# Optimization experiments

Measured on AMD Instinct MI355X. Metric: run time of the kernel, lower is better.

Reference implementation:

```python
import jax, jax.numpy as jnp
import numpy as np
from jax import lax

EPS = 1e-06


def _ema_scan(x, s):
    # x: [B, C, T]; s: [C] smoothing coeff in [0, 1]
    # Recurrence: y_0 = x_0; y_t = s * x_t + (1 - s) * y_{t-1}
    # Expressed as affine pairs (A_t, b_t) with y_t = A_t * y_{t-1} + b_t
    s_b = s[None, :, None]  # [1, C, 1]
    A0 = jnp.zeros_like(x[:, :, :1])
    A_rest = jnp.broadcast_to(1.0 - s_b, x[:, :, 1:].shape)
    A = jnp.concatenate([A0, A_rest], axis=2)
    b = jnp.concatenate([x[:, :, :1], s_b * x[:, :, 1:]], axis=2)

    def combine(c1, c2):
        a1, b1 = c1
        a2, b2 = c2
        return (a1 * a2, a2 * b1 + b2)

    _, ema = lax.associative_scan(combine, (A, b), axis=2)
    return ema


def setup_inputs() -> dict:
    key = jax.random.key(0)
    B, C, T = 32, 128, 16000
    kx, = jax.random.split(key, 1)
    x = jax.random.uniform(kx, (B, C, T), dtype=jnp.float32)
    alpha = jnp.ones((C,), dtype=jnp.float32) * 0.96
    delta = jnp.ones((C,), dtype=jnp.float32) * 2.0
    root = jnp.ones((C,), dtype=jnp.float32) * 2.0
    ema_weights = jnp.ones((C,), dtype=jnp.float32) * 0.04
    return {"x": x, "alpha": alpha, "delta": delta, "root": root, "ema_weights": ema_weights}


def reference(x, alpha, delta, root, ema_weights):
    # sPCEN: per-channel EMA smoother + power-law compression
    s = jnp.clip(ema_weights, 0.0, 1.0)
    ema = _ema_scan(x, s)  # [B, C, T]

    alpha_c = jnp.minimum(alpha, 1.0)[None, :, None]
    root_c = jnp.maximum(root, 1.0)[None, :, None]
    r = 1.0 / root_c
    d = delta[None, :, None]

    out = (x / (EPS + ema) ** alpha_c + d) ** r - d ** r
    return out
```

## Files before the change

kernel.cpp:

```cpp
#include <hip/hip_runtime.h>
#include <math.h>

#define T_LEN    16000
#define T_LEN4   4000
#define THREADS  256
#define CHUNK    16
#define TILE4    (THREADS * 4)
#define NT       4
#define EPS_F    1e-6f

__launch_bounds__(THREADS, 5)
__global__ void pcen_kernel(const float* __restrict__ x,
                            const float* __restrict__ alpha,
                            const float* __restrict__ delta,
                            const float* __restrict__ root,
                            const float* __restrict__ ema_w,
                            float* __restrict__ out, int C) {
    __shared__ float swA[2][4], swB[2][4];

    const int row  = blockIdx.x;
    const int c    = row % C;
    const int tid  = threadIdx.x;
    const int lane = tid & 63;
    const int wave = tid >> 6;

    const float s   = fminf(fmaxf(ema_w[c], 0.0f), 1.0f);
    const float q   = 1.0f - s;
    const float a_c = fminf(alpha[c], 1.0f);
    const float r   = 1.0f / fmaxf(root[c], 1.0f);
    const float d   = delta[c];
    const float dr  = powf(d, r);
    const float q16 = powf(q, (float)CHUNK);
    const bool  sqrt_path = (r == 0.5f);

    const float4* x4 = (const float4*)(x   + (size_t)row * T_LEN);
    float4*       o4 = (float4*)      (out + (size_t)row * T_LEN);

    float e_carry = 0.0f;

    auto loadt = [&](int t, float4& r0, float4& r1, float4& r2, float4& r3) {
        const int b = t * TILE4 + tid * 4;
        if (b < T_LEN4) { r0 = x4[b]; r1 = x4[b+1]; r2 = x4[b+2]; r3 = x4[b+3]; }
        else            { r0 = r1 = r2 = r3 = make_float4(1.f, 1.f, 1.f, 1.f); }
    };

    auto body = [&](int t, float4& c0, float4& c1, float4& c2, float4& c3,
                    bool pref, float4& n0, float4& n1, float4& n2, float4& n3) {
        const int  base4 = t * TILE4 + tid * 4;
        const bool valid = (base4 < T_LEN4);
        const int  p     = t & 1;

        float xv[CHUNK] = { c0.x, c0.y, c0.z, c0.w,  c1.x, c1.y, c1.z, c1.w,
                            c2.x, c2.y, c2.z, c2.w,  c3.x, c3.y, c3.z, c3.w };

        if (pref) loadt(t + 1, n0, n1, n2, n3);

        const bool ft = (t == 0) && (tid == 0);
        float la = ft ? 0.0f  : q16;
        float lb = ft ? xv[0] : s * xv[0];
        #pragma unroll
        for (int j = 1; j < CHUNK; ++j) lb = fmaf(q, lb, s * xv[j]);

        #pragma unroll
        for (int off = 1; off < 64; off <<= 1) {
            float ua = __shfl_up(la, off);
            float ub = __shfl_up(lb, off);
            if (lane >= off) { lb = fmaf(la, ub, lb); la *= ua; }
        }
        if (lane == 63) { swA[p][wave] = la; swB[p][wave] = lb; }

        asm volatile("s_waitcnt lgkmcnt(0)" ::: "memory");
        __builtin_amdgcn_s_barrier();

        float pa = 1.0f, pb = 0.0f;
        #pragma unroll
        for (int w = 0; w < 3; ++w)
            if (w < wave) { pb = fmaf(swA[p][w], pb, swB[p][w]); pa *= swA[p][w]; }

        float ea = __shfl_up(la, 1);
        float eb = __shfl_up(lb, 1);
        float a_ex, b_ex;
        if (lane == 0) { a_ex = pa;      b_ex = pb; }
        else           { a_ex = pa * ea; b_ex = fmaf(ea, pb, eb); }
        float e = fmaf(a_ex, e_carry, b_ex);

        float ta = 1.0f, tb = 0.0f;
        #pragma unroll
        for (int w = 0; w < 4; ++w) { tb = fmaf(swA[p][w], tb, swB[p][w]); ta *= swA[p][w]; }
        e_carry = fmaf(ta, e_carry, tb);

        if (valid) {
            if (sqrt_path) {
                #pragma unroll
                for (int j = 0; j < CHUNK; ++j) {
                    float xvj = xv[j];
                    e = (ft && j == 0) ? xvj : fmaf(q, e, s * xvj);
                    float lge = log2f(EPS_F + e);
                    float v   = xvj * exp2f(-a_c * lge);
                    xv[j] = sqrtf(v + d) - dr;
                }
            } else {
                #pragma unroll
                for (int j = 0; j < CHUNK; ++j) {
                    float xvj = xv[j];
                    e = (ft && j == 0) ? xvj : fmaf(q, e, s * xvj);
                    float lge = log2f(EPS_F + e);
                    float v   = xvj * exp2f(-a_c * lge);
                    xv[j] = exp2f(r * log2f(v + d)) - dr;
                }
            }
            o4[base4 + 0] = make_float4(xv[ 0], xv[ 1], xv[ 2], xv[ 3]);
            o4[base4 + 1] = make_float4(xv[ 4], xv[ 5], xv[ 6], xv[ 7]);
            o4[base4 + 2] = make_float4(xv[ 8], xv[ 9], xv[10], xv[11]);
            o4[base4 + 3] = make_float4(xv[12], xv[13], xv[14], xv[15]);
        }
    };

    float4 a0, a1, a2, a3, b0, b1, b2, b3;
    loadt(0, a0, a1, a2, a3);
    body(0, a0, a1, a2, a3, true,  b0, b1, b2, b3);
    body(1, b0, b1, b2, b3, true,  a0, a1, a2, a3);
    body(2, a0, a1, a2, a3, true,  b0, b1, b2, b3);
    body(3, b0, b1, b2, b3, false, a0, a1, a2, a3);
}

extern "C" void kernel_launch(void* const* d_in, const int* in_sizes, int n_in,
                              void* d_out, int out_size, void* d_ws, size_t ws_size,
                              hipStream_t stream) {
    const float* x     = (const float*)d_in[0];
    const float* alpha = (const float*)d_in[1];
    const float* delta = (const float*)d_in[2];
    const float* root  = (const float*)d_in[3];
    const float* ema_w = (const float*)d_in[4];
    float* out = (float*)d_out;

    const int C    = in_sizes[1];
    const int rows = in_sizes[0] / T_LEN;

    pcen_kernel<<<rows, THREADS, 0, stream>>>(x, alpha, delta, root, ema_w, out, C);
}
```

Baseline: 449.1 us.

## Assign one wavefront per row to remove block barriers and LDS exchange

Each row is now handled by a single 64-lane wavefront that walks 16 tiles sequentially, where before a 256-thread block split each row over 4 tiles. The cross-wave LDS exchange and s_barrier on every tile go away, and the tile carry is taken by a shuffle from lane 63. The price is a longer serial chain per wave (16 tiles instead of 4) and a quarter as many blocks, with launch bounds lowered from 5 to 4. The more the kernel is bound by memory bandwidth, the less the longer chain should matter.

```diff
diff --git a/kernel.cpp b/kernel.cpp
--- a/kernel.cpp
+++ b/kernel.cpp
@@ -4,25 +4,21 @@
 #define T_LEN    16000
 #define T_LEN4   4000
 #define THREADS  256
-#define CHUNK    16
-#define TILE4    (THREADS * 4)
-#define NT       4
+#define WTILE4   256
+#define NTILES   16
 #define EPS_F    1e-6f
 
-__launch_bounds__(THREADS, 5)
+__launch_bounds__(THREADS, 4)
 __global__ void pcen_kernel(const float* __restrict__ x,
                             const float* __restrict__ alpha,
                             const float* __restrict__ delta,
                             const float* __restrict__ root,
                             const float* __restrict__ ema_w,
-                            float* __restrict__ out, int C) {
-    __shared__ float swA[2][4], swB[2][4];
-
-    const int row  = blockIdx.x;
-    const int c    = row % C;
-    const int tid  = threadIdx.x;
-    const int lane = tid & 63;
-    const int wave = tid >> 6;
+                            float* __restrict__ out, int C, int rows) {
+    const int lane = threadIdx.x & 63;
+    const int row  = blockIdx.x * (THREADS / 64) + (threadIdx.x >> 6);
+    if (row >= rows) return;
+    const int c = row % C;
 
     const float s   = fminf(fmaxf(ema_w[c], 0.0f), 1.0f);
     const float q   = 1.0f - s;
@@ -30,7 +26,7 @@
     const float r   = 1.0f / fmaxf(root[c], 1.0f);
     const float d   = delta[c];
     const float dr  = powf(d, r);
-    const float q16 = powf(q, (float)CHUNK);
+    const float q16 = powf(q, 16.0f);
     const bool  sqrt_path = (r == 0.5f);
 
     const float4* x4 = (const float4*)(x   + (size_t)row * T_LEN);
@@ -39,27 +35,25 @@
     float e_carry = 0.0f;
 
     auto loadt = [&](int t, float4& r0, float4& r1, float4& r2, float4& r3) {
-        const int b = t * TILE4 + tid * 4;
-        if (b < T_LEN4) { r0 = x4[b]; r1 = x4[b+1]; r2 = x4[b+2]; r3 = x4[b+3]; }
-        else            { r0 = r1 = r2 = r3 = make_float4(1.f, 1.f, 1.f, 1.f); }
+        const int b4 = t * WTILE4 + lane * 4;
+        if (b4 < T_LEN4) { r0 = x4[b4]; r1 = x4[b4+1]; r2 = x4[b4+2]; r3 = x4[b4+3]; }
+        else             { r0 = r1 = r2 = r3 = make_float4(1.f, 1.f, 1.f, 1.f); }
     };
 
     auto body = [&](int t, float4& c0, float4& c1, float4& c2, float4& c3,
                     bool pref, float4& n0, float4& n1, float4& n2, float4& n3) {
-        const int  base4 = t * TILE4 + tid * 4;
-        const bool valid = (base4 < T_LEN4);
-        const int  p     = t & 1;
-
-        float xv[CHUNK] = { c0.x, c0.y, c0.z, c0.w,  c1.x, c1.y, c1.z, c1.w,
-                            c2.x, c2.y, c2.z, c2.w,  c3.x, c3.y, c3.z, c3.w };
+        const int  b4    = t * WTILE4 + lane * 4;
+        const bool valid = (b4 < T_LEN4);
+        float xv[16] = { c0.x, c0.y, c0.z, c0.w,  c1.x, c1.y, c1.z, c1.w,
+                         c2.x, c2.y, c2.z, c2.w,  c3.x, c3.y, c3.z, c3.w };
 
         if (pref) loadt(t + 1, n0, n1, n2, n3);
 
-        const bool ft = (t == 0) && (tid == 0);
+        const bool ft = (t == 0) && (lane == 0);
         float la = ft ? 0.0f  : q16;
         float lb = ft ? xv[0] : s * xv[0];
         #pragma unroll
-        for (int j = 1; j < CHUNK; ++j) lb = fmaf(q, lb, s * xv[j]);
+        for (int j = 1; j < 16; ++j) lb = fmaf(q, lb, s * xv[j]);
 
         #pragma unroll
         for (int off = 1; off < 64; off <<= 1) {
@@ -67,32 +61,21 @@
             float ub = __shfl_up(lb, off);
             if (lane >= off) { lb = fmaf(la, ub, lb); la *= ua; }
         }
-        if (lane == 63) { swA[p][wave] = la; swB[p][wave] = lb; }
-
-        asm volatile("s_waitcnt lgkmcnt(0)" ::: "memory");
-        __builtin_amdgcn_s_barrier();
-
-        float pa = 1.0f, pb = 0.0f;
-        #pragma unroll
-        for (int w = 0; w < 3; ++w)
-            if (w < wave) { pb = fmaf(swA[p][w], pb, swB[p][w]); pa *= swA[p][w]; }
 
         float ea = __shfl_up(la, 1);
         float eb = __shfl_up(lb, 1);
-        float a_ex, b_ex;
-        if (lane == 0) { a_ex = pa;      b_ex = pb; }
-        else           { a_ex = pa * ea; b_ex = fmaf(ea, pb, eb); }
+        float a_ex = (lane == 0) ? 1.0f : ea;
+        float b_ex = (lane == 0) ? 0.0f : eb;
         float e = fmaf(a_ex, e_carry, b_ex);
 
-        float ta = 1.0f, tb = 0.0f;
-        #pragma unroll
-        for (int w = 0; w < 4; ++w) { tb = fmaf(swA[p][w], tb, swB[p][w]); ta *= swA[p][w]; }
+        float ta = __shfl(la, 63);
+        float tb = __shfl(lb, 63);
         e_carry = fmaf(ta, e_carry, tb);
 
         if (valid) {
             if (sqrt_path) {
                 #pragma unroll
-                for (int j = 0; j < CHUNK; ++j) {
+                for (int j = 0; j < 16; ++j) {
                     float xvj = xv[j];
                     e = (ft && j == 0) ? xvj : fmaf(q, e, s * xvj);
                     float lge = log2f(EPS_F + e);
@@ -101,7 +84,7 @@
                 }
             } else {
                 #pragma unroll
-                for (int j = 0; j < CHUNK; ++j) {
+                for (int j = 0; j < 16; ++j) {
                     float xvj = xv[j];
                     e = (ft && j == 0) ? xvj : fmaf(q, e, s * xvj);
                     float lge = log2f(EPS_F + e);
@@ -109,19 +92,20 @@
                     xv[j] = exp2f(r * log2f(v + d)) - dr;
                 }
             }
-            o4[base4 + 0] = make_float4(xv[ 0], xv[ 1], xv[ 2], xv[ 3]);
-            o4[base4 + 1] = make_float4(xv[ 4], xv[ 5], xv[ 6], xv[ 7]);
-            o4[base4 + 2] = make_float4(xv[ 8], xv[ 9], xv[10], xv[11]);
-            o4[base4 + 3] = make_float4(xv[12], xv[13], xv[14], xv[15]);
+            o4[b4 + 0] = make_float4(xv[ 0], xv[ 1], xv[ 2], xv[ 3]);
+            o4[b4 + 1] = make_float4(xv[ 4], xv[ 5], xv[ 6], xv[ 7]);
+            o4[b4 + 2] = make_float4(xv[ 8], xv[ 9], xv[10], xv[11]);
+            o4[b4 + 3] = make_float4(xv[12], xv[13], xv[14], xv[15]);
         }
     };
 
-    float4 a0, a1, a2, a3, b0, b1, b2, b3;
-    loadt(0, a0, a1, a2, a3);
-    body(0, a0, a1, a2, a3, true,  b0, b1, b2, b3);
-    body(1, b0, b1, b2, b3, true,  a0, a1, a2, a3);
-    body(2, a0, a1, a2, a3, true,  b0, b1, b2, b3);
-    body(3, b0, b1, b2, b3, false, a0, a1, a2, a3);
+    float4 A0, A1, A2, A3, B0, B1, B2, B3;
+    loadt(0, A0, A1, A2, A3);
+    #pragma unroll
+    for (int tt = 0; tt < NTILES; tt += 2) {
+        body(tt,     A0, A1, A2, A3, true,           B0, B1, B2, B3);
+        body(tt + 1, B0, B1, B2, B3, tt + 2 < NTILES, A0, A1, A2, A3);
+    }
 }
 
 extern "C" void kernel_launch(void* const* d_in, const int* in_sizes, int n_in,
@@ -136,6 +120,7 @@
 
     const int C    = in_sizes[1];
     const int rows = in_sizes[0] / T_LEN;
+    const int blocks = (rows + 3) / 4;
 
-    pcen_kernel<<<rows, THREADS, 0, stream>>>(x, alpha, delta, root, ema_w, out, C);
+    pcen_kernel<<<blocks, THREADS, 0, stream>>>(x, alpha, delta, root, ema_w, out, C, rows);
 }
```

Measured after the change: 470.7 us. 4.8% more time.
